# Optimization experiments

Hardware: AMD Instinct MI355X
Metric: run time of the kernel (lower is better)

## Reference

```python
import jax, jax.numpy as jnp
import numpy as np

SCALE = 64.0
MARGIN = 0.35
EPS = 1e-12  # torch F.normalize eps


def _l2norm(a, axis):
    n = jnp.sqrt(jnp.sum(a * a, axis=axis, keepdims=True))
    return a / jnp.maximum(n, EPS)


def setup_inputs() -> dict:
    key = jax.random.key(0)
    k1, k2, k3 = jax.random.split(key, 3)
    B, D, C = 512, 512, 100000
    x = jax.random.normal(k1, (B, D), dtype=jnp.float32)
    gt = jax.random.randint(k2, (B,), 0, C, dtype=jnp.int64)
    # kaiming_normal_ on [C, D]: std = sqrt(2 / fan_in) with fan_in = D
    wt = jax.random.normal(k3, (C, D), dtype=jnp.float32) * np.sqrt(2.0 / D)
    return {"x": x, "gt": gt, "wt": wt}


def reference(x, gt, wt):
    wt_norm = _l2norm(wt, axis=1)          # [C, D]
    x_norm = _l2norm(x, axis=1)            # [B, D]
    cos = jnp.einsum("bd,cd->bc", x_norm, wt_norm)  # [B, C]
    # margin only at target index (avoids materializing one-hot)
    b = jnp.arange(x.shape[0])
    margin_score = cos.at[b, gt].add(-MARGIN)
    logits = SCALE * margin_score
    logp = jax.nn.log_softmax(logits, axis=-1)
    nll = -logp[b, gt]
    return jnp.mean(nll)
```

## Files before the change

### kernel.cpp

```cpp
#include <hip/hip_runtime.h>
#include <hip/hip_bf16.h>

#define DIM 512
#define BATCH 512
#define CCLS 100000
#define BM 256
#define BN 128
#define NT 782

typedef __attribute__((ext_vector_type(4))) float f32x4;

__device__ __forceinline__ void async_copy16(const unsigned char* g, unsigned char* l) {
  __builtin_amdgcn_global_load_lds((const __attribute__((address_space(1))) void*)g,
                                   (__attribute__((address_space(3))) void*)l, 16, 0, 0);
}

__global__ __launch_bounds__(256) void rownorm_fp8(const float* __restrict__ wt,
                                                   const float* __restrict__ x,
                                                   unsigned char* __restrict__ wn,
                                                   unsigned char* __restrict__ xn) {
  int wave = threadIdx.x >> 6;
  int lane = threadIdx.x & 63;
  int row4 = blockIdx.x * 4 + wave;
  const float* in;
  unsigned char* out;
  int row;
  if (row4 < CCLS) { in = wt; out = wn; row = row4; }
  else             { in = x;  out = xn; row = row4 - CCLS; }
  const float4* src = (const float4*)(in + (size_t)row * DIM);
  float4 v0 = src[2 * lane];
  float4 v1 = src[2 * lane + 1];
  float ss = v0.x*v0.x + v0.y*v0.y + v0.z*v0.z + v0.w*v0.w
           + v1.x*v1.x + v1.y*v1.y + v1.z*v1.z + v1.w*v1.w;
  #pragma unroll
  for (int off = 32; off > 0; off >>= 1) ss += __shfl_xor(ss, off, 64);
  float r = 1.0f / fmaxf(sqrtf(ss), 1e-12f);
  int p0 = __builtin_amdgcn_cvt_pk_fp8_f32(v0.x * r, v0.y * r, 0, false);
  p0     = __builtin_amdgcn_cvt_pk_fp8_f32(v0.z * r, v0.w * r, p0, true);
  int p1 = __builtin_amdgcn_cvt_pk_fp8_f32(v1.x * r, v1.y * r, 0, false);
  p1     = __builtin_amdgcn_cvt_pk_fp8_f32(v1.z * r, v1.w * r, p1, true);
  ((int2*)(out + (size_t)row * DIM))[lane] = make_int2(p0, p1);
}

__global__ __launch_bounds__(512, 4) void cosface_gemm(
    const unsigned char* __restrict__ xn,
    const unsigned char* __restrict__ wn,
    const int* __restrict__ gt,
    float* __restrict__ partial,
    float* __restrict__ tgt) {
  __shared__ __align__(16) unsigned char lds_a[BM * 128];
  __shared__ __align__(16) unsigned char lds_b[BN * 128];
  __shared__ float lds_rowsum[BM];
  __shared__ int lds_gt[BM];

  const int tid = threadIdx.x;
  const int lane = tid & 63;
  const int w = tid >> 6;
  const int wm = w >> 1;
  const int wn_ = w & 1;
  const int mt = blockIdx.x;
  const int nt = blockIdx.y;

  if (tid < BM) {
    lds_rowsum[tid] = 0.f;
    lds_gt[tid] = gt[mt * BM + tid];
  }

  const unsigned char* ga[4];
  const unsigned char* gb[2];
  #pragma unroll
  for (int j = 0; j < 4; ++j) {
    int c = j * 512 + tid;
    int m = c >> 3;
    int qg = (c & 7) ^ (m & 7);
    ga[j] = xn + (size_t)(mt * BM + m) * DIM + qg * 16;
  }
  #pragma unroll
  for (int j = 0; j < 2; ++j) {
    int c = j * 512 + tid;
    int m = c >> 3;
    int qg = (c & 7) ^ (m & 7);
    int rowB = nt * BN + m;
    if (rowB >= CCLS) rowB = CCLS - 1;
    gb[j] = wn + (size_t)rowB * DIM + qg * 16;
  }

  f32x4 acc[4][4];
  #pragma unroll
  for (int i = 0; i < 4; ++i)
    #pragma unroll
    for (int j = 0; j < 4; ++j)
      acc[i][j] = (f32x4){0.f, 0.f, 0.f, 0.f};

  const int quad = lane >> 4;
  const int l15 = lane & 15;
  const int arow = wm * 64 + l15;
  const int brow = wn_ * 64 + l15;
  const int swA = arow & 7;
  const int swB = brow & 7;

  for (int kk = 0; kk < 4; ++kk) {
    #pragma unroll
    for (int j = 0; j < 4; ++j)
      async_copy16(ga[j] + kk * 128, &lds_a[(j * 512 + w * 64) * 16]);
    #pragma unroll
    for (int j = 0; j < 2; ++j)
      async_copy16(gb[j] + kk * 128, &lds_b[(j * 512 + w * 64) * 16]);
    __syncthreads();
    #pragma unroll
    for (int s = 0; s < 4; ++s) {
      int g = s * 4 + quad;
      int cs = g >> 1;
      int h = (g & 1) * 8;
      long long af[4], bf[4];
      #pragma unroll
      for (int i = 0; i < 4; ++i) {
        af[i] = *(const long long*)&lds_a[(arow + i * 16) * 128 + ((cs ^ swA) * 16) + h];
        bf[i] = *(const long long*)&lds_b[(brow + i * 16) * 128 + ((cs ^ swB) * 16) + h];
      }
      #pragma unroll
      for (int i = 0; i < 4; ++i)
        #pragma unroll
        for (int j = 0; j < 4; ++j)
          acc[i][j] = __builtin_amdgcn_mfma_f32_16x16x32_fp8_fp8(af[i], bf[j], acc[i][j], 0, 0, 0);
    }
    __syncthreads();
  }

  #pragma unroll
  for (int i = 0; i < 4; ++i) {
    #pragma unroll
    for (int reg = 0; reg < 4; ++reg) {
      int m_loc = wm * 64 + i * 16 + quad * 4 + reg;
      int m_g = mt * BM + m_loc;
      int gtm = lds_gt[m_loc];
      float s = 0.f;
      #pragma unroll
      for (int j = 0; j < 4; ++j) {
        int n_g = nt * BN + wn_ * 64 + j * 16 + l15;
        float logit = 64.f * acc[i][j][reg];
        if (n_g == gtm) {
          logit -= 64.f * 0.35f;
          tgt[m_g] = logit;
        }
        if (n_g < CCLS) s += __expf(logit - 64.f);
      }
      #pragma unroll
      for (int off = 1; off < 16; off <<= 1) s += __shfl_xor(s, off, 64);
      if (l15 == 0) atomicAdd(&lds_rowsum[m_loc], s);
    }
  }
  __syncthreads();
  if (tid < BM)
    partial[(size_t)(mt * BM + tid) * NT + nt] = lds_rowsum[tid];
}

__global__ __launch_bounds__(64) void nll_rows(const float* __restrict__ partial,
                                               const float* __restrict__ tgt,
                                               float* __restrict__ nll) {
  int m = blockIdx.x;
  int lane = threadIdx.x;
  const float* row = partial + (size_t)m * NT;
  float s = 0.f;
  for (int t = lane; t < NT; t += 64) s += row[t];
  #pragma unroll
  for (int off = 32; off > 0; off >>= 1) s += __shfl_xor(s, off, 64);
  if (lane == 0) nll[m] = (logf(s) + 64.f) - tgt[m];
}

__global__ __launch_bounds__(512) void reduce_mean(const float* __restrict__ nll,
                                                   float* __restrict__ out) {
  __shared__ float red[BATCH];
  int m = threadIdx.x;
  red[m] = nll[m];
  __syncthreads();
  for (int k = 256; k > 0; k >>= 1) {
    if (m < k) red[m] += red[m + k];
    __syncthreads();
  }
  if (m == 0) out[0] = red[0] * (1.0f / BATCH);
}

extern "C" void kernel_launch(void* const* d_in, const int* in_sizes, int n_in,
                              void* d_out, int out_size, void* d_ws, size_t ws_size,
                              hipStream_t stream) {
  const float* x  = (const float*)d_in[0];
  const int*   gt = (const int*)d_in[1];
  const float* wt = (const float*)d_in[2];
  float* out = (float*)d_out;

  char* ws = (char*)d_ws;
  unsigned char* wn = (unsigned char*)ws;
  unsigned char* xn = (unsigned char*)(ws + 51200000);
  float* partial    = (float*)(ws + 51462144);
  float* tgt        = (float*)(ws + 53063680);
  float* nll        = (float*)(ws + 53065728);

  rownorm_fp8<<<(CCLS + BATCH) / 4, 256, 0, stream>>>(wt, x, wn, xn);
  cosface_gemm<<<dim3(2, NT), 512, 0, stream>>>(xn, wn, gt, partial, tgt);
  nll_rows<<<BATCH, 64, 0, stream>>>(partial, tgt, nll);
  reduce_mean<<<1, BATCH, 0, stream>>>(nll, out);
}
```

Baseline: 348.7 us.

## Use MI355 scaled 16x16x128 fp8 MFMA and remap block order for L2 reuse

Replaces the 16x16x32 fp8 MFMA inner loop with the gfx950 scaled 16x16x128 f8f6f4 instruction, using unit scales, so each k-chunk of 128 takes one MFMA per output tile. Fragments are now loaded as two 16-byte LDS reads per row instead of several 8-byte reads. The 2D grid becomes a 1D grid with a swizzled mapping that places both M-tiles of a group of eight N-tiles next to each other, so weight tiles are more likely to be reused from cache. Address setup is also simplified. The risk is wrong results if the fragment layout does not match what the scaled MFMA expects.

Result: slower. 579.5 us (+66.2%).

```diff
diff --git a/kernel.cpp b/kernel.cpp
--- a/kernel.cpp
+++ b/kernel.cpp
@@ -9,6 +9,7 @@
 #define NT 782
 
 typedef __attribute__((ext_vector_type(4))) float f32x4;
+typedef __attribute__((ext_vector_type(8))) int i32x8;
 
 __device__ __forceinline__ void async_copy16(const unsigned char* g, unsigned char* l) {
   __builtin_amdgcn_global_load_lds((const __attribute__((address_space(1))) void*)g,
@@ -42,12 +43,26 @@
   ((int2*)(out + (size_t)row * DIM))[lane] = make_int2(p0, p1);
 }
 
+__device__ __forceinline__ i32x8 load_frag(const unsigned char* lds, int row,
+                                           int quad, int sw) {
+  const unsigned char* base = lds + row * 128;
+  int4 lo = *(const int4*)(base + (((quad * 2)     ^ sw) * 16));
+  int4 hi = *(const int4*)(base + (((quad * 2 + 1) ^ sw) * 16));
+  i32x8 f = {lo.x, lo.y, lo.z, lo.w, hi.x, hi.y, hi.z, hi.w};
+  return f;
+}
+
 __global__ __launch_bounds__(512, 4) void cosface_gemm(
     const unsigned char* __restrict__ xn,
     const unsigned char* __restrict__ wn,
     const int* __restrict__ gt,
     float* __restrict__ partial,
     float* __restrict__ tgt) {
+  const int b = blockIdx.x;
+  const int mt = (b >> 3) & 1;
+  const int nt = (b & 7) | ((b >> 4) << 3);
+  if (nt >= NT) return;
+
   __shared__ __align__(16) unsigned char lds_a[BM * 128];
   __shared__ __align__(16) unsigned char lds_b[BN * 128];
   __shared__ float lds_rowsum[BM];
@@ -58,31 +73,21 @@
   const int w = tid >> 6;
   const int wm = w >> 1;
   const int wn_ = w & 1;
-  const int mt = blockIdx.x;
-  const int nt = blockIdx.y;
 
   if (tid < BM) {
     lds_rowsum[tid] = 0.f;
     lds_gt[tid] = gt[mt * BM + tid];
   }
 
-  const unsigned char* ga[4];
+  const int m0 = tid >> 3;
+  const int qg0 = (tid & 7) ^ (m0 & 7);
+  const unsigned char* ga0 = xn + (size_t)(mt * BM + m0) * DIM + qg0 * 16;
   const unsigned char* gb[2];
   #pragma unroll
-  for (int j = 0; j < 4; ++j) {
-    int c = j * 512 + tid;
-    int m = c >> 3;
-    int qg = (c & 7) ^ (m & 7);
-    ga[j] = xn + (size_t)(mt * BM + m) * DIM + qg * 16;
-  }
-  #pragma unroll
   for (int j = 0; j < 2; ++j) {
-    int c = j * 512 + tid;
-    int m = c >> 3;
-    int qg = (c & 7) ^ (m & 7);
-    int rowB = nt * BN + m;
+    int rowB = nt * BN + j * 64 + m0;
     if (rowB >= CCLS) rowB = CCLS - 1;
-    gb[j] = wn + (size_t)rowB * DIM + qg * 16;
+    gb[j] = wn + (size_t)rowB * DIM + qg0 * 16;
   }
 
   f32x4 acc[4][4];
@@ -102,27 +107,23 @@
   for (int kk = 0; kk < 4; ++kk) {
     #pragma unroll
     for (int j = 0; j < 4; ++j)
-      async_copy16(ga[j] + kk * 128, &lds_a[(j * 512 + w * 64) * 16]);
+      async_copy16(ga0 + j * 64 * DIM + kk * 128, &lds_a[(j * 512 + w * 64) * 16]);
     #pragma unroll
     for (int j = 0; j < 2; ++j)
       async_copy16(gb[j] + kk * 128, &lds_b[(j * 512 + w * 64) * 16]);
     __syncthreads();
-    #pragma unroll
-    for (int s = 0; s < 4; ++s) {
-      int g = s * 4 + quad;
-      int cs = g >> 1;
-      int h = (g & 1) * 8;
-      long long af[4], bf[4];
+
+    i32x8 bf[4];
+    #pragma unroll
+    for (int j = 0; j < 4; ++j)
+      bf[j] = load_frag(lds_b, brow + j * 16, quad, swB);
+    #pragma unroll
+    for (int i = 0; i < 4; ++i) {
+      i32x8 af = load_frag(lds_a, arow + i * 16, quad, swA);
       #pragma unroll
-      for (int i = 0; i < 4; ++i) {
-        af[i] = *(const long long*)&lds_a[(arow + i * 16) * 128 + ((cs ^ swA) * 16) + h];
-        bf[i] = *(const long long*)&lds_b[(brow + i * 16) * 128 + ((cs ^ swB) * 16) + h];
-      }
-      #pragma unroll
-      for (int i = 0; i < 4; ++i)
-        #pragma unroll
-        for (int j = 0; j < 4; ++j)
-          acc[i][j] = __builtin_amdgcn_mfma_f32_16x16x32_fp8_fp8(af[i], bf[j], acc[i][j], 0, 0, 0);
+      for (int j = 0; j < 4; ++j)
+        acc[i][j] = __builtin_amdgcn_mfma_scale_f32_16x16x128_f8f6f4(
+            af, bf[j], acc[i][j], 0, 0, 0, 127, 0, 127);
     }
     __syncthreads();
   }
@@ -197,7 +198,7 @@
   float* nll        = (float*)(ws + 53065728);
 
   rownorm_fp8<<<(CCLS + BATCH) / 4, 256, 0, stream>>>(wt, x, wn, xn);
-  cosface_gemm<<<dim3(2, NT), 512, 0, stream>>>(xn, wn, gt, partial, tgt);
+  cosface_gemm<<<1568, 512, 0, stream>>>(xn, wn, gt, partial, tgt);
   nll_rows<<<BATCH, 64, 0, stream>>>(partial, tgt, nll);
   reduce_mean<<<1, BATCH, 0, stream>>>(nll, out);
 }
```
